# Optimization experiments

Measured on AMD Instinct MI355X. Metric: run time of the kernel, lower is better.

The kernel has to match this reference:

```python
import jax, jax.numpy as jnp
import numpy as np

K = 512   # number of automaton states
S = 64    # segment vocabulary size
BSZ = 512 # batch of sequences
T = 64    # sequence length
A_SCALE = 0.02  # keeps recurrence spectral radius < 1 for numerical stability


def setup_inputs() -> dict:
    key = jax.random.key(0)
    kA, kB, kC, kP, kT = jax.random.split(key, 5)
    A = A_SCALE * jax.random.normal(kA, (K, K), dtype=jnp.float32)
    B = jax.random.normal(kB, (K, S), dtype=jnp.float32)
    C = jax.random.normal(kC, (S, K), dtype=jnp.float32)
    pi_params = jax.random.normal(kP, (S, K), dtype=jnp.float32)
    init = jnp.zeros((K,), dtype=jnp.float32).at[0].set(1.0)  # default e_0 init
    tokens = jax.random.randint(kT, (BSZ, T), 0, S, dtype=jnp.int32)
    return {"A": A, "B": B, "C": C, "pi_params": pi_params, "init": init, "tokens": tokens}


def reference(A, B, C, pi_params, init, tokens):
    # Real-semiring SSM forward recurrence (SSM.forward with float dtype):
    #   u[t]    = phi[input[t]]                (phi = eye(S) -> one-hot, realized as gathers)
    #   proj[t] = u[t] @ pi                    (tier gating, sigmoid-constrained to [0,1])
    #   x[t+1]  = (1 - proj[t]) * x[t] + proj[t] * (A @ x[t] + B @ u[t])
    #   y[t]    = (C * pi) @ x[t]              (predicts token t from pre-update state)
    # log-likelihood per sequence = sum_t log_softmax(y[t])[token_t]
    pi = jax.nn.sigmoid(pi_params)          # (S, K)
    C_eff = C * pi                          # (S, K)
    Bt = B.T                                # (S, K): Bt[tok] == B @ one_hot(tok)
    bsz = tokens.shape[0]
    x0 = jnp.broadcast_to(init, (bsz, init.shape[0]))  # (B, K)

    def step(x, tok):
        proj = pi[tok]                      # (B, K)
        update = x @ A.T + Bt[tok]          # (B, K)
        x_new = (1.0 - proj) * x + proj * update
        logits = x @ C_eff.T                # (B, S): y[t] from x[t] (pre-update)
        logp = jax.nn.log_softmax(logits, axis=-1)
        ll_t = jnp.take_along_axis(logp, tok[:, None], axis=-1)[:, 0]  # (B,)
        return x_new, ll_t

    _, lls = jax.lax.scan(step, x0, tokens.T)  # lls: (T, B)
    return lls.sum(0)                          # (B,) per-sequence log-likelihood
```

## Files before the change

### kernel.cpp

```cpp
#include <hip/hip_runtime.h>

#define K_DIM 512
#define S_DIM 64
#define T_LEN 64
#define BW    16
#define NWG   32

typedef float f32x4 __attribute__((ext_vector_type(4)));
typedef float f32x2 __attribute__((ext_vector_type(2)));
typedef long  i64x2 __attribute__((ext_vector_type(2)));

__device__ __forceinline__ char f2fp8(float f) {
    return (char)__builtin_amdgcn_cvt_pk_fp8_f32(f, f, 0, false);
}
__device__ __forceinline__ unsigned pack4fp8(float a, float b, float c, float d) {
    unsigned v = __builtin_amdgcn_cvt_pk_fp8_f32(a, b, 0, false);
    v = __builtin_amdgcn_cvt_pk_fp8_f32(c, d, v, true);
    return v;
}

__global__ void ssm_prep(const float* __restrict__ A, const float* __restrict__ B,
                         const float* __restrict__ C, const float* __restrict__ Pp,
                         char* __restrict__ A8, char* __restrict__ C8,
                         f32x2* __restrict__ PPB) {
    int i = blockIdx.x * blockDim.x + threadIdx.x;
    int stride = gridDim.x * blockDim.x;
    for (int idx = i; idx < K_DIM * K_DIM; idx += stride)
        A8[idx] = f2fp8(A[idx]);
    for (int idx = i; idx < S_DIM * K_DIM; idx += stride) {
        int s = idx >> 9;
        int k = idx & (K_DIM - 1);
        float p = 1.0f / (1.0f + expf(-Pp[idx]));
        C8[idx] = f2fp8(C[idx] * p);
        PPB[idx] = (f32x2){p, p * B[k * S_DIM + s]};
    }
}

#define MFMA8(aj, bj, acc) acc = __builtin_amdgcn_mfma_f32_16x16x32_fp8_fp8(aj, bj, acc, 0, 0, 0)

#define LOADM(m) \
    i64x2 ga_##m = *(const i64x2*)(a8P0 + (m) * 64); \
    i64x2 gb_##m = *(const i64x2*)(a8P1 + (m) * 64); \
    i64x2 gc_##m = *(const i64x2*)(a8P2 + (m) * 64); \
    i64x2 gd_##m = *(const i64x2*)(a8P3 + (m) * 64);

#define COMPM(m) { \
    i64x2 xv = *(const i64x2*)&Xb8[lr][(m) * 64 + 16 * lg]; \
    MFMA8(ga_##m[0], xv[0], acc0); MFMA8(ga_##m[1], xv[1], acc0); \
    MFMA8(gb_##m[0], xv[0], acc1); MFMA8(gb_##m[1], xv[1], acc1); \
    MFMA8(gc_##m[0], xv[0], acc2); MFMA8(gc_##m[1], xv[1], acc2); \
    MFMA8(gd_##m[0], xv[0], acc3); MFMA8(gd_##m[1], xv[1], acc3); }

#define COMPML(m) { \
    i64x2 xv = *(const i64x2*)&Xb8[lr][(m) * 64 + 16 * lg]; \
    i64x2 f0 = *(const i64x2*)&Aq8[w][(m) - 4][0][l][0]; \
    i64x2 f1 = *(const i64x2*)&Aq8[w][(m) - 4][1][l][0]; \
    i64x2 f2 = *(const i64x2*)&Aq8[w][(m) - 4][2][l][0]; \
    i64x2 f3 = *(const i64x2*)&Aq8[w][(m) - 4][3][l][0]; \
    MFMA8(f0[0], xv[0], acc0); MFMA8(f0[1], xv[1], acc0); \
    MFMA8(f1[0], xv[0], acc1); MFMA8(f1[1], xv[1], acc1); \
    MFMA8(f2[0], xv[0], acc2); MFMA8(f2[1], xv[1], acc2); \
    MFMA8(f3[0], xv[0], acc3); MFMA8(f3[1], xv[1], acc3); }

#define LBAR asm volatile("s_waitcnt lgkmcnt(0)\ns_barrier" ::: "memory")

__global__ __launch_bounds__(512) __attribute__((amdgpu_waves_per_eu(2, 2)))
void ssm_main(
    const char*  __restrict__ A8,
    const char*  __restrict__ C8,
    const f32x2* __restrict__ PPB,
    const float* __restrict__ init,
    const int*   __restrict__ tokens,
    float*       __restrict__ out)
{
    __shared__ char  Aq8[8][4][4][64][16];
    __shared__ char  Xb8[BW][528];
    __shared__ float Lg[2][BW][68];
    __shared__ int   tokS[BW][T_LEN];

    const int tid = threadIdx.x;
    const int w  = tid >> 6;
    const int l  = tid & 63;
    const int lg = l >> 4;
    const int lr = l & 15;
    const int b0 = blockIdx.x * BW;

    for (int idx = tid; idx < BW * T_LEN; idx += 512) {
        int r = idx >> 6, t = idx & 63;
        tokS[r][t] = tokens[(b0 + r) * T_LEN + t];
    }
    for (int idx = tid; idx < BW * K_DIM; idx += 512) {
        int r = idx >> 9, k = idx & (K_DIM - 1);
        Xb8[r][k] = f2fp8(init[k]);
    }
    for (int idx = tid; idx < 8192; idx += 512) {
        int w2 = idx >> 10, rem = idx & 1023;
        int m2 = rem >> 8, rem2 = rem & 255;
        int q2 = rem2 >> 6, l2 = rem2 & 63;
        *(i64x2*)&Aq8[w2][m2][q2][l2][0] =
            *(const i64x2*)(A8 + (w2 * 64 + q2 * 16 + (l2 & 15)) * K_DIM
                            + (4 + m2) * 64 + (l2 >> 4) * 16);
    }
    float xm[4][4];
    #pragma unroll
    for (int nt = 0; nt < 4; ++nt) {
        #pragma unroll
        for (int e = 0; e < 4; ++e)
            xm[nt][e] = init[w * 64 + nt * 16 + 4 * lg + e];
    }

    const int sq = w & 3;
    const int kh = w >> 2;

    const char* a8P0 = A8 + (w * 64 +      lr) * K_DIM + 16 * lg;
    const char* a8P1 = A8 + (w * 64 + 16 + lr) * K_DIM + 16 * lg;
    const char* a8P2 = A8 + (w * 64 + 32 + lr) * K_DIM + 16 * lg;
    const char* a8P3 = A8 + (w * 64 + 48 + lr) * K_DIM + 16 * lg;
    const char* c8P  = C8 + (sq * 16 + lr) * K_DIM + kh * 256 + 16 * lg;

    float llacc = 0.0f;
    __syncthreads();

    for (int t = 0; t < T_LEN; ++t) {
        LOADM(0) LOADM(1)

        f32x4 lga = {0.f, 0.f, 0.f, 0.f};
        #pragma unroll
        for (int j = 0; j < 4; ++j) {
            i64x2 cv = *(const i64x2*)(c8P + j * 64);
            i64x2 xv = *(const i64x2*)&Xb8[lr][kh * 256 + j * 64 + 16 * lg];
            MFMA8(xv[0], cv[0], lga);
            MFMA8(xv[1], cv[1], lga);
        }
        #pragma unroll
        for (int e = 0; e < 4; ++e)
            Lg[kh][4 * lg + e][sq * 16 + lr] = lga[e];

        f32x4 acc0 = {0.f, 0.f, 0.f, 0.f};
        f32x4 acc1 = {0.f, 0.f, 0.f, 0.f};
        f32x4 acc2 = {0.f, 0.f, 0.f, 0.f};
        f32x4 acc3 = {0.f, 0.f, 0.f, 0.f};
        COMPM(0)  LOADM(2)
        COMPM(1)  LOADM(3)
        COMPM(2)
        COMPM(3)
        int mytok = tokS[lr][t];
        f32x4 ppv[4][2];
        #pragma unroll
        for (int nt = 0; nt < 4; ++nt) {
            const f32x2* pp = PPB + mytok * K_DIM + w * 64 + nt * 16 + 4 * lg;
            ppv[nt][0] = *(const f32x4*)(pp);
            ppv[nt][1] = *(const f32x4*)(pp + 2);
        }
        COMPML(4) COMPML(5) COMPML(6) COMPML(7)
        LBAR;

        #pragma unroll
        for (int nt = 0; nt < 4; ++nt) {
            f32x4 a = (nt == 0) ? acc0 : (nt == 1) ? acc1 : (nt == 2) ? acc2 : acc3;
            float nx0 = xm[nt][0] + ppv[nt][0][0] * (a[0] - xm[nt][0]) + ppv[nt][0][1];
            float nx1 = xm[nt][1] + ppv[nt][0][2] * (a[1] - xm[nt][1]) + ppv[nt][0][3];
            float nx2 = xm[nt][2] + ppv[nt][1][0] * (a[2] - xm[nt][2]) + ppv[nt][1][1];
            float nx3 = xm[nt][3] + ppv[nt][1][2] * (a[3] - xm[nt][3]) + ppv[nt][1][3];
            xm[nt][0] = nx0; xm[nt][1] = nx1; xm[nt][2] = nx2; xm[nt][3] = nx3;
            *(unsigned*)&Xb8[lr][w * 64 + nt * 16 + 4 * lg] = pack4fp8(nx0, nx1, nx2, nx3);
        }
        if (w < 4) {
            int b = w * 4 + (l >> 4);
            int i = l & 15;
            float v[4];
            #pragma unroll
            for (int c = 0; c < 4; ++c)
                v[c] = Lg[0][b][i * 4 + c] + Lg[1][b][i * 4 + c];
            float m = fmaxf(fmaxf(v[0], v[1]), fmaxf(v[2], v[3]));
            m = fmaxf(m, __shfl_xor(m, 1));
            m = fmaxf(m, __shfl_xor(m, 2));
            m = fmaxf(m, __shfl_xor(m, 4));
            m = fmaxf(m, __shfl_xor(m, 8));
            float sum = expf(v[0] - m) + expf(v[1] - m) + expf(v[2] - m) + expf(v[3] - m);
            sum += __shfl_xor(sum, 1);
            sum += __shfl_xor(sum, 2);
            sum += __shfl_xor(sum, 4);
            sum += __shfl_xor(sum, 8);
            int tok = tokS[b][t];
            float sel = (i == (tok >> 2)) ? v[tok & 3] : 0.0f;
            sel += __shfl_xor(sel, 1);
            sel += __shfl_xor(sel, 2);
            sel += __shfl_xor(sel, 4);
            sel += __shfl_xor(sel, 8);
            llacc += sel - m - logf(sum);
        }
        LBAR;
    }

    if (w < 4 && (l & 15) == 0)
        out[b0 + w * 4 + (l >> 4)] = llacc;
}

extern "C" void kernel_launch(void* const* d_in, const int* in_sizes, int n_in,
                              void* d_out, int out_size, void* d_ws, size_t ws_size,
                              hipStream_t stream) {
    const float* A  = (const float*)d_in[0];
    const float* B  = (const float*)d_in[1];
    const float* C  = (const float*)d_in[2];
    const float* Pp = (const float*)d_in[3];
    const float* init = (const float*)d_in[4];
    const int* tokens = (const int*)d_in[5];
    float* out = (float*)d_out;

    char*  A8  = (char*)d_ws;
    char*  C8  = (char*)d_ws + 262144;
    f32x2* PPB = (f32x2*)((char*)d_ws + 294912);

    ssm_prep<<<256, 256, 0, stream>>>(A, B, C, Pp, A8, C8, PPB);
    ssm_main<<<NWG, 512, 0, stream>>>(A8, C8, PPB, init, tokens, out);
}
```

Measured before the change: 177.6 us.

## Double-buffer logits and overlap log-softmax of previous step with matmul

Logits are now written to a double-buffered shared array indexed by step parity. The log-softmax for step t-1 is computed by waves 0-3 before the LDS-fed half of the A matmul, instead of after the state update. This moves the softmax off the serial tail between the two barriers, overlapping it with MFMA work from other waves. The cost is extra shared memory and a duplicated epilogue for the final step.

```diff
diff --git a/kernel.cpp b/kernel.cpp
--- a/kernel.cpp
+++ b/kernel.cpp
@@ -75,7 +75,7 @@
 {
     __shared__ char  Aq8[8][4][4][64][16];
     __shared__ char  Xb8[BW][528];
-    __shared__ float Lg[2][BW][68];
+    __shared__ float Lg[2][2][BW][68];
     __shared__ int   tokS[BW][T_LEN];
 
     const int tid = threadIdx.x;
@@ -122,6 +122,8 @@
     __syncthreads();
 
     for (int t = 0; t < T_LEN; ++t) {
+        const int p = t & 1;
+
         LOADM(0) LOADM(1)
 
         f32x4 lga = {0.f, 0.f, 0.f, 0.f};
@@ -134,7 +136,7 @@
         }
         #pragma unroll
         for (int e = 0; e < 4; ++e)
-            Lg[kh][4 * lg + e][sq * 16 + lr] = lga[e];
+            Lg[p][kh][4 * lg + e][sq * 16 + lr] = lga[e];
 
         f32x4 acc0 = {0.f, 0.f, 0.f, 0.f};
         f32x4 acc1 = {0.f, 0.f, 0.f, 0.f};
@@ -152,26 +154,14 @@
             ppv[nt][0] = *(const f32x4*)(pp);
             ppv[nt][1] = *(const f32x4*)(pp + 2);
         }
-        COMPML(4) COMPML(5) COMPML(6) COMPML(7)
-        LBAR;
-
-        #pragma unroll
-        for (int nt = 0; nt < 4; ++nt) {
-            f32x4 a = (nt == 0) ? acc0 : (nt == 1) ? acc1 : (nt == 2) ? acc2 : acc3;
-            float nx0 = xm[nt][0] + ppv[nt][0][0] * (a[0] - xm[nt][0]) + ppv[nt][0][1];
-            float nx1 = xm[nt][1] + ppv[nt][0][2] * (a[1] - xm[nt][1]) + ppv[nt][0][3];
-            float nx2 = xm[nt][2] + ppv[nt][1][0] * (a[2] - xm[nt][2]) + ppv[nt][1][1];
-            float nx3 = xm[nt][3] + ppv[nt][1][2] * (a[3] - xm[nt][3]) + ppv[nt][1][3];
-            xm[nt][0] = nx0; xm[nt][1] = nx1; xm[nt][2] = nx2; xm[nt][3] = nx3;
-            *(unsigned*)&Xb8[lr][w * 64 + nt * 16 + 4 * lg] = pack4fp8(nx0, nx1, nx2, nx3);
-        }
-        if (w < 4) {
+
+        if (t > 0 && w < 4) {
             int b = w * 4 + (l >> 4);
             int i = l & 15;
             float v[4];
             #pragma unroll
             for (int c = 0; c < 4; ++c)
-                v[c] = Lg[0][b][i * 4 + c] + Lg[1][b][i * 4 + c];
+                v[c] = Lg[1 - p][0][b][i * 4 + c] + Lg[1 - p][1][b][i * 4 + c];
             float m = fmaxf(fmaxf(v[0], v[1]), fmaxf(v[2], v[3]));
             m = fmaxf(m, __shfl_xor(m, 1));
             m = fmaxf(m, __shfl_xor(m, 2));
@@ -182,7 +172,7 @@
             sum += __shfl_xor(sum, 2);
             sum += __shfl_xor(sum, 4);
             sum += __shfl_xor(sum, 8);
-            int tok = tokS[b][t];
+            int tok = tokS[b][t - 1];
             float sel = (i == (tok >> 2)) ? v[tok & 3] : 0.0f;
             sel += __shfl_xor(sel, 1);
             sel += __shfl_xor(sel, 2);
@@ -190,11 +180,51 @@
             sel += __shfl_xor(sel, 8);
             llacc += sel - m - logf(sum);
         }
+
+        COMPML(4) COMPML(5) COMPML(6) COMPML(7)
         LBAR;
-    }
-
-    if (w < 4 && (l & 15) == 0)
-        out[b0 + w * 4 + (l >> 4)] = llacc;
+
+        #pragma unroll
+        for (int nt = 0; nt < 4; ++nt) {
+            f32x4 a = (nt == 0) ? acc0 : (nt == 1) ? acc1 : (nt == 2) ? acc2 : acc3;
+            float nx0 = xm[nt][0] + ppv[nt][0][0] * (a[0] - xm[nt][0]) + ppv[nt][0][1];
+            float nx1 = xm[nt][1] + ppv[nt][0][2] * (a[1] - xm[nt][1]) + ppv[nt][0][3];
+            float nx2 = xm[nt][2] + ppv[nt][1][0] * (a[2] - xm[nt][2]) + ppv[nt][1][1];
+            float nx3 = xm[nt][3] + ppv[nt][1][2] * (a[3] - xm[nt][3]) + ppv[nt][1][3];
+            xm[nt][0] = nx0; xm[nt][1] = nx1; xm[nt][2] = nx2; xm[nt][3] = nx3;
+            *(unsigned*)&Xb8[lr][w * 64 + nt * 16 + 4 * lg] = pack4fp8(nx0, nx1, nx2, nx3);
+        }
+        LBAR;
+    }
+
+    if (w < 4) {
+        int b = w * 4 + (l >> 4);
+        int i = l & 15;
+        float v[4];
+        #pragma unroll
+        for (int c = 0; c < 4; ++c)
+            v[c] = Lg[1][0][b][i * 4 + c] + Lg[1][1][b][i * 4 + c];
+        float m = fmaxf(fmaxf(v[0], v[1]), fmaxf(v[2], v[3]));
+        m = fmaxf(m, __shfl_xor(m, 1));
+        m = fmaxf(m, __shfl_xor(m, 2));
+        m = fmaxf(m, __shfl_xor(m, 4));
+        m = fmaxf(m, __shfl_xor(m, 8));
+        float sum = expf(v[0] - m) + expf(v[1] - m) + expf(v[2] - m) + expf(v[3] - m);
+        sum += __shfl_xor(sum, 1);
+        sum += __shfl_xor(sum, 2);
+        sum += __shfl_xor(sum, 4);
+        sum += __shfl_xor(sum, 8);
+        int tok = tokS[b][T_LEN - 1];
+        float sel = (i == (tok >> 2)) ? v[tok & 3] : 0.0f;
+        sel += __shfl_xor(sel, 1);
+        sel += __shfl_xor(sel, 2);
+        sel += __shfl_xor(sel, 4);
+        sel += __shfl_xor(sel, 8);
+        llacc += sel - m - logf(sum);
+
+        if ((l & 15) == 0)
+            out[b0 + w * 4 + (l >> 4)] = llacc;
+    }
 }
 
 extern "C" void kernel_launch(void* const* d_in, const int* in_sizes, int n_in,
```

Result: faster. 164.6 us (-7.3%).
